# Kernel optimization log

Hardware: AMD Instinct MI355X
Metric: run time of the kernel (lower is better)

Reference implementation:

```python
import jax, jax.numpy as jnp
import numpy as np

N = 16384            # mesh vertices at full resolution (level 3)
DEG = 8              # avg nonzeros per Laplacian row
F_IN = 3
F_HID = 128
LOCAL_LAYERS = 15
LEVEL_N = [N >> (3 - l) for l in range(4)]  # [2048, 4096, 8192, 16384]


def setup_inputs():
    key = jax.random.key(0)
    ks = iter(jax.random.split(key, 48))
    d = {}
    d['inputs'] = jax.random.normal(next(ks), (1, N, F_IN), dtype=jnp.float32)
    d['mask0'] = jnp.ones((1, N, 1), jnp.float32)
    d['mask1'] = jnp.ones((1, N, 1), jnp.float32)
    for l, n in enumerate(LEVEL_N):
        e = DEG * n
        d[f'lap{l}_rows'] = jnp.sort(jax.random.randint(next(ks), (e,), 0, n, dtype=jnp.int32))
        d[f'lap{l}_cols'] = jax.random.randint(next(ks), (e,), 0, n, dtype=jnp.int32)
        d[f'lap{l}_vals'] = 0.25 * jax.random.normal(next(ks), (e,), dtype=jnp.float32)
    e = DEG * N
    d['L_rows'] = jnp.sort(jax.random.randint(next(ks), (e,), 0, N, dtype=jnp.int32))
    d['L_cols'] = jax.random.randint(next(ks), (e,), 0, N, dtype=jnp.int32)
    d['L_vals'] = 0.25 * jax.random.normal(next(ks), (e,), dtype=jnp.float32)
    s_in = 0.577   # ~1/sqrt(F_IN)
    s_h = 0.0625   # 1/sqrt(2*F_HID)
    d['g_conv1_W'] = s_in * jax.random.normal(next(ks), (F_IN, F_HID), dtype=jnp.float32)
    d['g_conv1_b'] = jnp.zeros((F_HID,), jnp.float32)
    d['g_down_W'] = s_h * jax.random.normal(next(ks), (3, 2, 2 * F_HID, F_HID), dtype=jnp.float32)
    d['g_down_b'] = jnp.zeros((3, 2, F_HID), jnp.float32)
    d['g_lap0_W'] = s_h * jax.random.normal(next(ks), (2, 2 * F_HID, F_HID), dtype=jnp.float32)
    d['g_lap0_b'] = jnp.zeros((2, F_HID), jnp.float32)
    d['g_up_W'] = s_h * jax.random.normal(next(ks), (3, 2, 2 * F_HID, F_HID), dtype=jnp.float32)
    d['g_up_b'] = jnp.zeros((3, 2, F_HID), jnp.float32)
    d['g_conv2_W'] = s_h * jax.random.normal(next(ks), (F_HID, 2), dtype=jnp.float32)
    d['g_conv2_b'] = jnp.zeros((2,), jnp.float32)
    d['l_conv1_W'] = s_in * jax.random.normal(next(ks), (F_IN, F_HID), dtype=jnp.float32)
    d['l_conv1_b'] = jnp.zeros((F_HID,), jnp.float32)
    d['l_rn_W'] = s_h * jax.random.normal(next(ks), (LOCAL_LAYERS, 2, 2 * F_HID, F_HID), dtype=jnp.float32)
    d['l_rn_b'] = jnp.zeros((LOCAL_LAYERS, 2, F_HID), jnp.float32)
    d['l_conv2_W'] = s_h * jax.random.normal(next(ks), (F_HID, 1), dtype=jnp.float32)
    d['l_conv2_b'] = jnp.zeros((1,), jnp.float32)
    return d


def _spmm(rows, cols, vals, x):
    # y = L @ x for an n x n COO Laplacian; x: [1, n, f] (batch=1, sparse mm path)
    y = jax.ops.segment_sum(vals[:, None] * x[0, cols, :], rows, num_segments=x.shape[1])
    return y[None]


def _lap_block(lap, x, Ws, bs):
    # _LapResNet2 (num_outputs == num_inputs == 128): elu -> cat([x, Lx]) -> 1x1 conv, residual
    inp = x
    for j in range(Ws.shape[0]):
        x = jax.nn.elu(x)
        x = jnp.concatenate([x, _spmm(lap[0], lap[1], lap[2], x)], axis=-1) @ Ws[j] + bs[j]
    return x + inp


def _avg_block(mask, x, Ws, bs):
    # _AvgResNet2: elu -> cat([x, masked global average]) -> 1x1 conv, residual
    inp = x
    denom = jnp.sum(mask, axis=1, keepdims=True)
    for j in range(Ws.shape[0]):
        x = jax.nn.elu(x)
        avg = jnp.sum(x * mask, axis=1, keepdims=True) / denom
        x = jnp.concatenate([x, jnp.broadcast_to(avg, x.shape)], axis=-1) @ Ws[j] + bs[j]
    return x + inp


def _maxpool2(x):
    # MaxPool1d(2, stride=2) along the node dim
    b, n, f = x.shape
    return x.reshape(b, n // 2, 2, f).max(axis=2)


def _forward(inputs, mask0, mask1, lap0_vals, lap1_vals, lap2_vals, lap3_vals, L_vals,
             g_conv1_W, g_conv1_b, g_down_W, g_down_b, g_lap0_W, g_lap0_b,
             g_up_W, g_up_b, g_conv2_W, g_conv2_b,
             l_conv1_W, l_conv1_b, l_rn_W, l_rn_b, l_conv2_W, l_conv2_b,
             lap0_rows, lap0_cols, lap1_rows, lap1_cols, lap2_rows, lap2_cols,
             lap3_rows, lap3_cols, L_rows, L_cols):
    laps = [(lap0_rows, lap0_cols, lap0_vals), (lap1_rows, lap1_cols, lap1_vals),
            (lap2_rows, lap2_cols, lap2_vals), (lap3_rows, lap3_cols, lap3_vals)]
    # ----- global net: EfficientCascade (naive max-pool cascade, 4 levels) -----
    # (mask0 is only max-pooled in torch; _LapResNet2 ignores it, so it does not affect math)
    x = inputs @ g_conv1_W + g_conv1_b
    down = []
    for k, i in enumerate((3, 2, 1)):
        down.append(x)
        x = _lap_block(laps[i], x, g_down_W[k], g_down_b[k])
        x = _maxpool2(x)
    x = _lap_block(laps[0], x, g_lap0_W, g_lap0_b)
    for i in (1, 2, 3):
        x = jnp.repeat(x, 2, axis=1)      # F.interpolate(scale_factor=2), nearest
        x = x + down[-i]                  # channels equal -> plain residual add
        x = _lap_block(laps[i], x, g_up_W[i - 1], g_up_b[i - 1])
    swg = jax.nn.elu(x) @ g_conv2_W + g_conv2_b + inputs[:, :, :2]  # + repeating_expand(inputs, 2)
    # ----- local net: LapDeepModel, 15 alternating Lap / global-avg resblocks -----
    L = (L_rows, L_cols, L_vals)
    y = inputs @ l_conv1_W + l_conv1_b
    for i in range(LOCAL_LAYERS):
        if i % 2 == 0:
            y = _lap_block(L, y, l_rn_W[i], l_rn_b[i])
        else:
            y = _avg_block(mask1, y, l_rn_W[i], l_rn_b[i])
    score_local = jax.nn.elu(y) @ l_conv2_W + l_conv2_b + inputs[:, :, :1]
    # ----- combine -----
    score_global = swg[:, :, :1]
    weight_global = jax.nn.sigmoid(swg[:, :, :-1])  # out_features=1 -> same first channel
    score_final = weight_global * score_global + (1.0 - weight_global) * score_local
    return jnp.concatenate([score_global, score_local, score_final], axis=1)


def reference(inputs, mask0, mask1, lap0_rows, lap0_cols, lap0_vals,
              lap1_rows, lap1_cols, lap1_vals, lap2_rows, lap2_cols, lap2_vals,
              lap3_rows, lap3_cols, lap3_vals, L_rows, L_cols, L_vals,
              g_conv1_W, g_conv1_b, g_down_W, g_down_b, g_lap0_W, g_lap0_b,
              g_up_W, g_up_b, g_conv2_W, g_conv2_b,
              l_conv1_W, l_conv1_b, l_rn_W, l_rn_b, l_conv2_W, l_conv2_b):
    return _forward(inputs, mask0, mask1, lap0_vals, lap1_vals, lap2_vals, lap3_vals, L_vals,
                    g_conv1_W, g_conv1_b, g_down_W, g_down_b, g_lap0_W, g_lap0_b,
                    g_up_W, g_up_b, g_conv2_W, g_conv2_b,
                    l_conv1_W, l_conv1_b, l_rn_W, l_rn_b, l_conv2_W, l_conv2_b,
                    lap0_rows, lap0_cols, lap1_rows, lap1_cols, lap2_rows, lap2_cols,
                    lap3_rows, lap3_cols, L_rows, L_cols)
```

## Files before the change

kernel.cpp:

```cpp
#include <hip/hip_runtime.h>

#define F 128
#define SPAD 136
#define NR 16

typedef __attribute__((ext_vector_type(8))) short short8;
typedef __attribute__((ext_vector_type(4))) float f32x4;
typedef unsigned long long ull;

__device__ __forceinline__ float elu_f(float x) {
    return x > 0.f ? x : __expf(x) - 1.f;
}
__device__ __forceinline__ ushort f2bf(float x) {
    unsigned u = __float_as_uint(x);
    u = (u + 0x7FFFu + ((u >> 16) & 1u)) >> 16;
    return (ushort)u;
}
__device__ __forceinline__ float bf2f(ushort u) {
    return __uint_as_float((unsigned)u << 16);
}
__device__ __forceinline__ void bfma8(float* a, float v, short8 u) {
#pragma unroll
    for (int i = 0; i < 8; ++i) a[i] += v * bf2f((ushort)u[i]);
}

struct SetupArgs {
    const float* ws0; const float* ws1; const float* ws2; const float* ws3;
    ushort* wd0; ushort* wd1; ushort* wd2; ushort* wd3;
    const int* rows0; const int* rows1; const int* rows2; const int* rows3; const int* rows4;
    int* rp0; int* rp1; int* rp2; int* rp3; int* rp4;
    const float* mask; float* den; float* acc;
    const float* in; const float* Wg; const float* bg; const float* Wl; const float* bl;
    ushort* og; ushort* eg; ushort* ol; ushort* el;
};

__global__ __launch_bounds__(256) void setup_conv1(SetupArgs s) {
    __shared__ ushort tile[16384];
    int b = blockIdx.x, t = threadIdx.x;
    if (b >= 274) {
        int id = (b - 274) * 256 + t;
        int r = id >> 7, c = id & 127;
        float x0 = s.in[r * 3 + 0], x1 = s.in[r * 3 + 1], x2 = s.in[r * 3 + 2];
        float g = x0 * s.Wg[c] + x1 * s.Wg[F + c] + x2 * s.Wg[2 * F + c] + s.bg[c];
        float lo = x0 * s.Wl[c] + x1 * s.Wl[F + c] + x2 * s.Wl[2 * F + c] + s.bl[c];
        s.og[id] = f2bf(g);  s.eg[id] = f2bf(elu_f(g));
        s.ol[id] = f2bf(lo); s.el[id] = f2bf(elu_f(lo));
    } else if (b < 88) {
        const float* src; ushort* dst; int lb;
        if (b < 12)      { src = s.ws0; dst = s.wd0; lb = b; }
        else if (b < 16) { src = s.ws1; dst = s.wd1; lb = b - 12; }
        else if (b < 28) { src = s.ws2; dst = s.wd2; lb = b - 16; }
        else             { src = s.ws3; dst = s.wd3; lb = b - 28; }
        src += (size_t)lb * 16384; dst += (size_t)lb * 16384;
        for (int idx = t; idx < 16384; idx += 256) {
            int k = idx >> 7, nn = idx & 127;
            int kt = k >> 5, lq = (k >> 3) & 3, j = k & 7;
            int wv = nn >> 5, ct = (nn >> 4) & 1, cc = nn & 15;
            tile[((((kt * 4 + wv) * 2 + ct) * 64 + lq * 16 + cc)) * 8 + j] = f2bf(src[idx]);
        }
        __syncthreads();
        ull* td = (ull*)dst; const ull* ts = (const ull*)tile;
        for (int i = t; i < 4096; i += 256) td[i] = ts[i];
    } else if (b < 273) {
        int tid = (b - 88) * 256 + t;
        const int ns[5] = {2048, 4096, 8192, 16384, 16384};
        const int es[5] = {16384, 32768, 65536, 131072, 131072};
        const int* rowsA[5] = {s.rows0, s.rows1, s.rows2, s.rows3, s.rows4};
        int* rpA[5] = {s.rp0, s.rp1, s.rp2, s.rp3, s.rp4};
        int base = 0;
        for (int lv = 0; lv < 5; ++lv) {
            int cnt = ns[lv] + 1;
            if (tid < base + cnt) {
                int r = tid - base;
                const int* rows = rowsA[lv]; int e = es[lv];
                int lo = 0, hi = e;
                while (lo < hi) { int mid = (lo + hi) >> 1; if (rows[mid] < r) lo = mid + 1; else hi = mid; }
                rpA[lv][r] = lo;
                return;
            }
            base += cnt;
        }
    } else {
        __shared__ float red[256];
        float ssum = 0.f;
        for (int i = t; i < 16384; i += 256) ssum += s.mask[i];
        red[t] = ssum; __syncthreads();
        for (int st = 128; st > 0; st >>= 1) { if (t < st) red[t] += red[t + st]; __syncthreads(); }
        if (t == 0) s.den[0] = red[0];
        for (int i = t; i < 14336; i += 256) s.acc[i] = 0.f;
    }
}

struct LArgs {
    const ushort* EA; const ushort* RES; ushort* OUT; ushort* EAOUT;
    const int* rowptr; const int* cols; const float* vals;
    const ushort* Wp; const float* bias;
    const float* accin; const float* den;
    const float* mask; float* accout;
    ushort* EO; ushort* EE; const ushort* SKIP;
    int epi;
    int fin;
    const float* Finp; const ushort* FEB0;
    const float* FgW2; const float* Fgb2; const float* FlW2; const float* Flb2;
    float* Fout;
};

__device__ __forceinline__ void layer_body(const LArgs& a, int blk, ushort* SS, float* FS) {
    const int t = threadIdx.x;
    const int rbase = blk * NR;
    const int w = t >> 6, l = t & 63;
    const int cl = l & 15, lq = l >> 4;
    const bool lap = (a.rowptr != nullptr);
    const bool avg = (a.accin != nullptr);

    if (lap) {
        const int grp = t >> 4, l16 = t & 15;
        const int lbase = l & ~15;
        const short8* EA8 = (const short8*)a.EA;
        const int row = rbase + grp;
        const int e0 = a.rowptr[row], e1 = a.rowptr[row + 1];
        float acc0[8];
#pragma unroll
        for (int i = 0; i < 8; ++i) acc0[i] = 0.f;
        int myc = 0; float myv = 0.f;
        if (e0 + l16 < e1) { myc = a.cols[e0 + l16]; myv = a.vals[e0 + l16]; }
#pragma unroll 1
        for (int base = e0; base < e1; base += 16) {
            int nc = 0; float nv = 0.f;
            {
                int en = base + 16 + l16;
                if (en < e1) { nc = a.cols[en]; nv = a.vals[en]; }
            }
#pragma unroll
            for (int half = 0; half < 2; ++half) {
                int hb = base + half * 8;
                if (hb < e1) {
                    int cnt = e1 - hb; if (cnt > 8) cnt = 8;
                    int cc[8];
#pragma unroll
                    for (int k = 0; k < 8; ++k) cc[k] = __shfl(myc, lbase + half * 8 + k, 64);
                    short8 ua[8];
#pragma unroll
                    for (int k = 0; k < 8; ++k)
                        if (k < cnt) ua[k] = EA8[(size_t)cc[k] * 16 + l16];
#pragma unroll
                    for (int k = 0; k < 8; ++k)
                        if (k < cnt) {
                            float v = __shfl(myv, lbase + half * 8 + k, 64);
                            bfma8(acc0, v, ua[k]);
                        }
                }
            }
            myc = nc; myv = nv;
        }
        short8 s0;
#pragma unroll
        for (int i = 0; i < 8; ++i) s0[i] = (short)f2bf(acc0[i]);
        *(short8*)(&SS[grp * SPAD + l16 * 8]) = s0;
        __syncthreads();
    } else if (avg) {
        if (t < 128) {
            float s = 0.f;
#pragma unroll
            for (int r = 0; r < 8; ++r) s += a.accin[r * 128 + t];
            SS[t] = f2bf(s / a.den[0]);
        }
        __syncthreads();
    }

    short8 afrag[4];
    {
        const ushort* ear = a.EA + (size_t)(rbase + cl) * F + lq * 8;
#pragma unroll
        for (int kt = 0; kt < 4; ++kt) afrag[kt] = *(const short8*)(ear + kt * 32);
    }

    f32x4 accA, accB;
#pragma unroll
    for (int i = 0; i < 4; ++i) { accA[i] = 0.f; accB[i] = 0.f; }
#pragma unroll
    for (int kt = 0; kt < 4; ++kt) {
        short8 b0 = *(const short8*)(a.Wp + (size_t)((((kt * 4 + w) * 2 + 0) * 64 + l) * 8));
        short8 b1 = *(const short8*)(a.Wp + (size_t)((((kt * 4 + w) * 2 + 1) * 64 + l) * 8));
        accA = __builtin_amdgcn_mfma_f32_16x16x32_bf16(afrag[kt], b0, accA, 0, 0, 0);
        accB = __builtin_amdgcn_mfma_f32_16x16x32_bf16(afrag[kt], b1, accB, 0, 0, 0);
    }
    if (lap || avg) {
        const ushort* esr = lap ? &SS[cl * SPAD + lq * 8] : &SS[lq * 8];
#pragma unroll
        for (int kt = 0; kt < 4; ++kt) {
            short8 aa = *(const short8*)(esr + kt * 32);
            short8 b0 = *(const short8*)(a.Wp + 16384 + (size_t)((((kt * 4 + w) * 2 + 0) * 64 + l) * 8));
            short8 b1 = *(const short8*)(a.Wp + 16384 + (size_t)((((kt * 4 + w) * 2 + 1) * 64 + l) * 8));
            accA = __builtin_amdgcn_mfma_f32_16x16x32_bf16(aa, b0, accA, 0, 0, 0);
            accB = __builtin_amdgcn_mfma_f32_16x16x32_bf16(aa, b1, accB, 0, 0, 0);
        }
    }

    const int col0 = w * 32 + cl, col1 = w * 32 + 16 + cl;
    const float bv0 = a.bias[col0], bv1 = a.bias[col1];
    float outv[8];
#pragma unroll
    for (int reg = 0; reg < 4; ++reg) {
        int r = lq * 4 + reg;
        size_t rg = (size_t)(rbase + r);
        float v0 = accA[reg] + bv0;
        float v1 = accB[reg] + bv1;
        if (a.RES) { v0 += bf2f(a.RES[rg * F + col0]); v1 += bf2f(a.RES[rg * F + col1]); }
        outv[reg] = v0; outv[4 + reg] = v1;
        if (a.OUT) { a.OUT[rg * F + col0] = f2bf(v0); a.OUT[rg * F + col1] = f2bf(v1); }
        if (a.EAOUT) { a.EAOUT[rg * F + col0] = f2bf(elu_f(v0)); a.EAOUT[rg * F + col1] = f2bf(elu_f(v1)); }
    }
    if (a.accout) {
        float p0 = 0.f, p1 = 0.f;
#pragma unroll
        for (int reg = 0; reg < 4; ++reg) {
            float mk = a.mask[rbase + lq * 4 + reg];
            p0 += elu_f(outv[reg]) * mk;
            p1 += elu_f(outv[4 + reg]) * mk;
        }
        p0 += __shfl_xor(p0, 16, 64); p0 += __shfl_xor(p0, 32, 64);
        p1 += __shfl_xor(p1, 16, 64); p1 += __shfl_xor(p1, 32, 64);
        if (l < 16) {
            atomicAdd(a.accout + (blk & 7) * 128 + w * 32 + l, p0);
            atomicAdd(a.accout + (blk & 7) * 128 + w * 32 + 16 + l, p1);
        }
    }
    if (a.epi == 1) {
        int rb2 = rbase >> 1;
#pragma unroll
        for (int ct = 0; ct < 2; ++ct)
#pragma unroll
            for (int e2 = 0; e2 < 2; ++e2) {
                float pv = fmaxf(outv[ct * 4 + e2 * 2], outv[ct * 4 + e2 * 2 + 1]);
                size_t idx = (size_t)(rb2 + lq * 2 + e2) * F + (ct ? col1 : col0);
                a.EO[idx] = f2bf(pv);
                a.EE[idx] = f2bf(elu_f(pv));
            }
    } else if (a.epi == 2) {
#pragma unroll
        for (int ct = 0; ct < 2; ++ct)
#pragma unroll
            for (int reg = 0; reg < 4; ++reg) {
                int r = lq * 4 + reg;
                size_t R0 = (size_t)(2 * (rbase + r)) * F + (ct ? col1 : col0);
                float v0 = outv[ct * 4 + reg] + bf2f(a.SKIP[R0]);
                float v1 = outv[ct * 4 + reg] + bf2f(a.SKIP[R0 + F]);
                a.EO[R0] = f2bf(v0);     a.EO[R0 + F] = f2bf(v1);
                a.EE[R0] = f2bf(elu_f(v0)); a.EE[R0 + F] = f2bf(elu_f(v1));
            }
    }
    if (a.fin) {
        __syncthreads();
        if (t < 32) FS[t] = 0.f;
        __syncthreads();
#pragma unroll
        for (int ct = 0; ct < 2; ++ct) {
            float lw = a.FlW2[ct ? col1 : col0];
#pragma unroll
            for (int reg = 0; reg < 4; ++reg)
                atomicAdd(&FS[lq * 4 + reg], elu_f(outv[ct * 4 + reg]) * lw);
        }
        for (int idx = t; idx < 16 * 128; idx += 256) {
            int r = idx >> 7, cc = idx & 127;
            atomicAdd(&FS[16 + r], bf2f(a.FEB0[(size_t)(rbase + r) * F + cc]) * a.FgW2[2 * cc]);
        }
        __syncthreads();
        if (t < 16) {
            int rg = rbase + t;
            float base = a.Finp[rg * 3 + 0];
            float sg = FS[16 + t] + a.Fgb2[0] + base;
            float sl = FS[t] + a.Flb2[0] + base;
            float wg = 1.f / (1.f + __expf(-sg));
            a.Fout[rg] = sg;
            a.Fout[16384 + rg] = sl;
            a.Fout[32768 + rg] = wg * sg + (1.f - wg) * sl;
        }
    }
}

__global__ __launch_bounds__(256)
void dual_layer(LArgs A, LArgs B, int nA) {
    __shared__ ushort SS[NR * SPAD];
    __shared__ float FS[64];
    bool isA = (int)blockIdx.x < nA;
    const LArgs& a = isA ? A : B;
    int blk = isA ? blockIdx.x : blockIdx.x - nA;
    layer_body(a, blk, SS, FS);
}

extern "C" void kernel_launch(void* const* d_in, const int* in_sizes, int n_in,
                              void* d_out, int out_size, void* d_ws, size_t ws_size,
                              hipStream_t stream) {
    (void)in_sizes; (void)n_in; (void)out_size; (void)ws_size;
    const float* inputs = (const float*)d_in[0];
    const float* mask1  = (const float*)d_in[2];
    const int*   lrows[5] = {(const int*)d_in[3], (const int*)d_in[6], (const int*)d_in[9],
                             (const int*)d_in[12], (const int*)d_in[15]};
    const int*   lcols[5] = {(const int*)d_in[4], (const int*)d_in[7], (const int*)d_in[10],
                             (const int*)d_in[13], (const int*)d_in[16]};
    const float* lvals[5] = {(const float*)d_in[5], (const float*)d_in[8], (const float*)d_in[11],
                             (const float*)d_in[14], (const float*)d_in[17]};
    const float* gW1 = (const float*)d_in[18];
    const float* gb1 = (const float*)d_in[19];
    const float* gdW = (const float*)d_in[20];
    const float* gdb = (const float*)d_in[21];
    const float* glW = (const float*)d_in[22];
    const float* glb = (const float*)d_in[23];
    const float* guW = (const float*)d_in[24];
    const float* gub = (const float*)d_in[25];
    const float* gW2 = (const float*)d_in[26];
    const float* gb2 = (const float*)d_in[27];
    const float* lW1 = (const float*)d_in[28];
    const float* lb1 = (const float*)d_in[29];
    const float* lrW = (const float*)d_in[30];
    const float* lrb = (const float*)d_in[31];
    const float* lW2 = (const float*)d_in[32];
    const float* lb2 = (const float*)d_in[33];
    float* out = (float*)d_out;

    const int N = 16384;
    const int nlev[5] = {2048, 4096, 8192, 16384, 16384};

    char* ws = (char*)d_ws;
    size_t off = 0;
    auto alloc = [&](size_t bytes) -> char* {
        char* p = ws + off;
        off = (off + bytes + 255) & ~(size_t)255;
        return p;
    };
    ushort* BUF0 = (ushort*)alloc((size_t)N * F * 2);
    ushort* GU2  = (ushort*)alloc((size_t)N * F * 2);
    ushort* G2   = (ushort*)alloc((size_t)N * F * 2);
    ushort* D8   = (ushort*)alloc((size_t)8192 * F * 2);
    ushort* D4   = (ushort*)alloc((size_t)4096 * F * 2);
    ushort* D2   = (ushort*)alloc((size_t)2048 * F * 2);
    ushort* LB   = (ushort*)alloc((size_t)N * F * 2);
    ushort* EB0 = (ushort*)alloc((size_t)N * F * 2);
    ushort* EG1 = (ushort*)alloc((size_t)N * F * 2);
    ushort* EG2 = (ushort*)alloc((size_t)N * F * 2);
    ushort* ED8 = (ushort*)alloc((size_t)8192 * F * 2);
    ushort* ED4 = (ushort*)alloc((size_t)4096 * F * 2);
    ushort* ED2 = (ushort*)alloc((size_t)2048 * F * 2);
    ushort* LE1 = (ushort*)alloc((size_t)N * F * 2);
    ushort* LE2 = (ushort*)alloc((size_t)N * F * 2);
    int* rp[5];
    for (int i = 0; i < 5; ++i) rp[i] = (int*)alloc((size_t)(nlev[i] + 1) * 4);
    float* ACC = (float*)alloc((size_t)14 * 8 * 128 * 4);
    float* DEN = (float*)alloc(4);
    ushort* Pd = (ushort*)alloc((size_t)12 * 16384 * 2);
    ushort* Pl = (ushort*)alloc((size_t)4  * 16384 * 2);
    ushort* Pu = (ushort*)alloc((size_t)12 * 16384 * 2);
    ushort* Pr = (ushort*)alloc((size_t)60 * 16384 * 2);

    SetupArgs sa;
    sa.ws0 = gdW; sa.ws1 = glW; sa.ws2 = guW; sa.ws3 = lrW;
    sa.wd0 = Pd;  sa.wd1 = Pl;  sa.wd2 = Pu;  sa.wd3 = Pr;
    sa.rows0 = lrows[0]; sa.rows1 = lrows[1]; sa.rows2 = lrows[2];
    sa.rows3 = lrows[3]; sa.rows4 = lrows[4];
    sa.rp0 = rp[0]; sa.rp1 = rp[1]; sa.rp2 = rp[2]; sa.rp3 = rp[3]; sa.rp4 = rp[4];
    sa.mask = mask1; sa.den = DEN; sa.acc = ACC;
    sa.in = inputs; sa.Wg = gW1; sa.bg = gb1; sa.Wl = lW1; sa.bl = lb1;
    sa.og = BUF0; sa.eg = EB0; sa.ol = LB; sa.el = LE1;
    setup_conv1<<<274 + 8192, 256, 0, stream>>>(sa);

    const size_t PSZ = 2 * 16384;

    auto mkL = [&](const ushort* ea, const ushort* res, ushort* o, ushort* eao,
                   int lv, const ushort* wp, const float* bias, float* accout,
                   int epi, ushort* eo, ushort* ee, const ushort* skip,
                   const float* accin, int fin) {
        LArgs x;
        x.EA = ea; x.RES = res; x.OUT = o; x.EAOUT = eao;
        x.rowptr = (lv >= 0) ? rp[lv] : nullptr;
        x.cols = (lv >= 0) ? lcols[lv] : nullptr;
        x.vals = (lv >= 0) ? lvals[lv] : nullptr;
        x.Wp = wp; x.bias = bias;
        x.accin = accin; x.den = DEN;
        x.mask = mask1; x.accout = accout;
        x.EO = eo; x.EE = ee; x.SKIP = skip; x.epi = epi;
        x.fin = fin;
        x.Finp = inputs; x.FEB0 = EB0;
        x.FgW2 = gW2; x.Fgb2 = gb2; x.FlW2 = lW2; x.Flb2 = lb2; x.Fout = out;
        return x;
    };

    LArgs gs[14]; int gn[14];
    gs[0]  = mkL(EB0, 0, 0, EG1, 3, Pd + 0 * PSZ, gdb + 0,   0, 0, 0, 0, 0, 0, 0);  gn[0]  = 16384;
    gs[1]  = mkL(EG1, BUF0, 0, 0, 3, Pd + 1 * PSZ, gdb + 128, 0, 1, D8, ED8, 0, 0, 0); gn[1] = 16384;
    gs[2]  = mkL(ED8, 0, 0, EG1, 2, Pd + 2 * PSZ, gdb + 256, 0, 0, 0, 0, 0, 0, 0);  gn[2]  = 8192;
    gs[3]  = mkL(EG1, D8, 0, 0, 2, Pd + 3 * PSZ, gdb + 384, 0, 1, D4, ED4, 0, 0, 0); gn[3]  = 8192;
    gs[4]  = mkL(ED4, 0, 0, EG1, 1, Pd + 4 * PSZ, gdb + 512, 0, 0, 0, 0, 0, 0, 0);  gn[4]  = 4096;
    gs[5]  = mkL(EG1, D4, 0, 0, 1, Pd + 5 * PSZ, gdb + 640, 0, 1, D2, ED2, 0, 0, 0); gn[5]  = 4096;
    gs[6]  = mkL(ED2, 0, 0, EG1, 0, Pl + 0 * PSZ, glb + 0,   0, 0, 0, 0, 0, 0, 0);  gn[6]  = 2048;
    gs[7]  = mkL(EG1, D2, 0, 0, 0, Pl + 1 * PSZ, glb + 128, 0, 2, GU2, EG2, D4, 0, 0); gn[7] = 2048;
    gs[8]  = mkL(EG2, 0, 0, EG1, 1, Pu + 0 * PSZ, gub + 0,   0, 0, 0, 0, 0, 0, 0);  gn[8]  = 4096;
    gs[9]  = mkL(EG1, GU2, 0, 0, 1, Pu + 1 * PSZ, gub + 128, 0, 2, G2, EG2, D8, 0, 0); gn[9] = 4096;
    gs[10] = mkL(EG2, 0, 0, EG1, 2, Pu + 2 * PSZ, gub + 256, 0, 0, 0, 0, 0, 0, 0);  gn[10] = 8192;
    gs[11] = mkL(EG1, G2, 0, 0, 2, Pu + 3 * PSZ, gub + 384, 0, 2, GU2, EG2, BUF0, 0, 0); gn[11] = 8192;
    gs[12] = mkL(EG2, 0, 0, EG1, 3, Pu + 4 * PSZ, gub + 512, 0, 0, 0, 0, 0, 0, 0);  gn[12] = 16384;
    gs[13] = mkL(EG1, GU2, 0, EB0, 3, Pu + 5 * PSZ, gub + 640, 0, 0, 0, 0, 0, 0, 0); gn[13] = 16384;

    const int NB_LOC = N / NR;
    int gi = 0;
    auto launchLap = [&](const LArgs& loc) {
        if (gi < 14) {
            int na = gn[gi] / NR;
            dual_layer<<<na + NB_LOC, 256, 0, stream>>>(gs[gi], loc, na);
            ++gi;
        } else {
            dual_layer<<<NB_LOC, 256, 0, stream>>>(loc, loc, NB_LOC);
        }
    };

    for (int i = 0; i < 15; ++i) {
        const ushort* P1 = Pr + (size_t)(2 * i) * PSZ;
        const ushort* P2 = Pr + (size_t)(2 * i + 1) * PSZ;
        const float* b1 = lrb + (size_t)i * 256;
        const float* b2 = b1 + 128;
        if ((i & 1) == 0) {
            LArgs s1 = mkL(LE1, 0, 0, LE2, 4, P1, b1, 0, 0, 0, 0, 0, 0, 0);
            float* accout = (i <= 12) ? (ACC + (size_t)i * 1024) : nullptr;
            int fin = (i == 14);
            LArgs s2 = mkL(LE2, LB, fin ? nullptr : LB, fin ? nullptr : LE1, 4,
                           P2, b2, accout, 0, 0, 0, 0, 0, fin);
            launchLap(s1);
            launchLap(s2);
        } else {
            LArgs s1 = mkL(LE1, 0, 0, LE2, -1, P1, b1, ACC + (size_t)i * 1024,
                           0, 0, 0, 0, ACC + (size_t)(i - 1) * 1024, 0);
            LArgs s2 = mkL(LE2, LB, LB, LE1, -1, P2, b2, 0,
                           0, 0, 0, 0, ACC + (size_t)i * 1024, 0);
            launchLap(s1);
            launchLap(s2);
        }
    }
}
```

Baseline: 596.0 us.

## Sort full-resolution Laplacian rows by degree to balance per-block SpMM work

Adds a small kernel that builds a permutation of the 16384-row level-3 and local Laplacian rows, bucketed by nonzero count in descending order. The affected global and local layers then process rows in that order and gather and scatter through the permutation for activations, residuals, mask and final outputs. The aim is that rows sharing a block and wavefront have similar edge counts, so fewer lanes sit idle in the gather loop. The cost is one extra launch, an indirection load per row, and row accesses that are no longer contiguous across a block.

```diff
diff --git a/kernel.cpp b/kernel.cpp
--- a/kernel.cpp
+++ b/kernel.cpp
@@ -91,9 +91,38 @@
     }
 }
 
+struct PermArgs { const int* rpA; int* permA; const int* rpB; int* permB; int n; };
+
+__global__ __launch_bounds__(1024) void build_perm(PermArgs p) {
+    const int* rp = blockIdx.x ? p.rpB : p.rpA;
+    int* perm = blockIdx.x ? p.permB : p.permA;
+    const int n = p.n;
+    __shared__ int hist[64];
+    __shared__ int base[64];
+    int t = threadIdx.x;
+    if (t < 64) hist[t] = 0;
+    __syncthreads();
+    for (int r = t; r < n; r += 1024) {
+        int d = rp[r + 1] - rp[r]; if (d > 63) d = 63;
+        atomicAdd(&hist[d], 1);
+    }
+    __syncthreads();
+    if (t == 0) {
+        int acc = 0;
+        for (int d = 63; d >= 0; --d) { base[d] = acc; acc += hist[d]; }
+    }
+    __syncthreads();
+    for (int r = t; r < n; r += 1024) {
+        int d = rp[r + 1] - rp[r]; if (d > 63) d = 63;
+        int pos = atomicAdd(&base[d], 1);
+        perm[pos] = r;
+    }
+}
+
 struct LArgs {
     const ushort* EA; const ushort* RES; ushort* OUT; ushort* EAOUT;
     const int* rowptr; const int* cols; const float* vals;
+    const int* perm;
     const ushort* Wp; const float* bias;
     const float* accin; const float* den;
     const float* mask; float* accout;
@@ -112,12 +141,13 @@
     const int cl = l & 15, lq = l >> 4;
     const bool lap = (a.rowptr != nullptr);
     const bool avg = (a.accin != nullptr);
+    const int* pm = a.perm;
 
     if (lap) {
         const int grp = t >> 4, l16 = t & 15;
         const int lbase = l & ~15;
         const short8* EA8 = (const short8*)a.EA;
-        const int row = rbase + grp;
+        const int row = pm ? pm[rbase + grp] : (rbase + grp);
         const int e0 = a.rowptr[row], e1 = a.rowptr[row + 1];
         float acc0[8];
 #pragma unroll
@@ -170,7 +200,8 @@
 
     short8 afrag[4];
     {
-        const ushort* ear = a.EA + (size_t)(rbase + cl) * F + lq * 8;
+        const int rowA = pm ? pm[rbase + cl] : (rbase + cl);
+        const ushort* ear = a.EA + (size_t)rowA * F + lq * 8;
 #pragma unroll
         for (int kt = 0; kt < 4; ++kt) afrag[kt] = *(const short8*)(ear + kt * 32);
     }
@@ -203,7 +234,7 @@
 #pragma unroll
     for (int reg = 0; reg < 4; ++reg) {
         int r = lq * 4 + reg;
-        size_t rg = (size_t)(rbase + r);
+        size_t rg = (size_t)(pm ? pm[rbase + r] : (rbase + r));
         float v0 = accA[reg] + bv0;
         float v1 = accB[reg] + bv1;
         if (a.RES) { v0 += bf2f(a.RES[rg * F + col0]); v1 += bf2f(a.RES[rg * F + col1]); }
@@ -215,7 +246,9 @@
         float p0 = 0.f, p1 = 0.f;
 #pragma unroll
         for (int reg = 0; reg < 4; ++reg) {
-            float mk = a.mask[rbase + lq * 4 + reg];
+            int r = lq * 4 + reg;
+            int rg = pm ? pm[rbase + r] : (rbase + r);
+            float mk = a.mask[rg];
             p0 += elu_f(outv[reg]) * mk;
             p1 += elu_f(outv[4 + reg]) * mk;
         }
@@ -263,11 +296,12 @@
         }
         for (int idx = t; idx < 16 * 128; idx += 256) {
             int r = idx >> 7, cc = idx & 127;
-            atomicAdd(&FS[16 + r], bf2f(a.FEB0[(size_t)(rbase + r) * F + cc]) * a.FgW2[2 * cc]);
+            int rg = pm ? pm[rbase + r] : (rbase + r);
+            atomicAdd(&FS[16 + r], bf2f(a.FEB0[(size_t)rg * F + cc]) * a.FgW2[2 * cc]);
         }
         __syncthreads();
         if (t < 16) {
-            int rg = rbase + t;
+            int rg = pm ? pm[rbase + t] : (rbase + t);
             float base = a.Finp[rg * 3 + 0];
             float sg = FS[16 + t] + a.Fgb2[0] + base;
             float sl = FS[t] + a.Flb2[0] + base;
@@ -348,6 +382,8 @@
     for (int i = 0; i < 5; ++i) rp[i] = (int*)alloc((size_t)(nlev[i] + 1) * 4);
     float* ACC = (float*)alloc((size_t)14 * 8 * 128 * 4);
     float* DEN = (float*)alloc(4);
+    int* P3 = (int*)alloc((size_t)N * 4);
+    int* P4 = (int*)alloc((size_t)N * 4);
     ushort* Pd = (ushort*)alloc((size_t)12 * 16384 * 2);
     ushort* Pl = (ushort*)alloc((size_t)4  * 16384 * 2);
     ushort* Pu = (ushort*)alloc((size_t)12 * 16384 * 2);
@@ -364,6 +400,12 @@
     sa.og = BUF0; sa.eg = EB0; sa.ol = LB; sa.el = LE1;
     setup_conv1<<<274 + 8192, 256, 0, stream>>>(sa);
 
+    PermArgs pa;
+    pa.rpA = rp[3]; pa.permA = P3;
+    pa.rpB = rp[4]; pa.permB = P4;
+    pa.n = N;
+    build_perm<<<2, 1024, 0, stream>>>(pa);
+
     const size_t PSZ = 2 * 16384;
 
     auto mkL = [&](const ushort* ea, const ushort* res, ushort* o, ushort* eao,
@@ -375,6 +417,7 @@
         x.rowptr = (lv >= 0) ? rp[lv] : nullptr;
         x.cols = (lv >= 0) ? lcols[lv] : nullptr;
         x.vals = (lv >= 0) ? lvals[lv] : nullptr;
+        x.perm = nullptr;
         x.Wp = wp; x.bias = bias;
         x.accin = accin; x.den = DEN;
         x.mask = mask1; x.accout = accout;
@@ -400,6 +443,7 @@
     gs[11] = mkL(EG1, G2, 0, 0, 2, Pu + 3 * PSZ, gub + 384, 0, 2, GU2, EG2, BUF0, 0, 0); gn[11] = 8192;
     gs[12] = mkL(EG2, 0, 0, EG1, 3, Pu + 4 * PSZ, gub + 512, 0, 0, 0, 0, 0, 0, 0);  gn[12] = 16384;
     gs[13] = mkL(EG1, GU2, 0, EB0, 3, Pu + 5 * PSZ, gub + 640, 0, 0, 0, 0, 0, 0, 0); gn[13] = 16384;
+    gs[0].perm = P3; gs[12].perm = P3; gs[13].perm = P3;
 
     const int NB_LOC = N / NR;
     int gi = 0;
@@ -420,10 +464,12 @@
         const float* b2 = b1 + 128;
         if ((i & 1) == 0) {
             LArgs s1 = mkL(LE1, 0, 0, LE2, 4, P1, b1, 0, 0, 0, 0, 0, 0, 0);
+            s1.perm = P4;
             float* accout = (i <= 12) ? (ACC + (size_t)i * 1024) : nullptr;
             int fin = (i == 14);
             LArgs s2 = mkL(LE2, LB, fin ? nullptr : LB, fin ? nullptr : LE1, 4,
                            P2, b2, accout, 0, 0, 0, 0, 0, fin);
+            s2.perm = P4;
             launchLap(s1);
             launchLap(s2);
         } else {
```

Measured after the change: 663.3 us. 1.11x slower.

## Fuse paired avg-pool residual layers into one kernel with a grid-wide barrier

Applied to the files above, without the earlier changes.

For odd local layers, the two launches (first half producing the masked mean, second half consuming it) are merged into one fused kernel. Blocks spin on an agent-scope atomic counter until every local block has added its partial sums, then run the second GEMM from shared memory. This removes a kernel launch and a global round trip of the intermediate activation per pair, and it co-schedules global-branch blocks in the same grid. It relies on all NB_LOC blocks being resident at once, otherwise the spin barrier deadlocks. Counters are zeroed in the setup kernel.

```diff
diff --git a/kernel.cpp b/kernel.cpp
--- a/kernel.cpp
+++ b/kernel.cpp
@@ -30,6 +30,7 @@
     const int* rows0; const int* rows1; const int* rows2; const int* rows3; const int* rows4;
     int* rp0; int* rp1; int* rp2; int* rp3; int* rp4;
     const float* mask; float* den; float* acc;
+    int* cnt;
     const float* in; const float* Wg; const float* bg; const float* Wl; const float* bl;
     ushort* og; ushort* eg; ushort* ol; ushort* el;
 };
@@ -88,6 +89,7 @@
         for (int st = 128; st > 0; st >>= 1) { if (t < st) red[t] += red[t + st]; __syncthreads(); }
         if (t == 0) s.den[0] = red[0];
         for (int i = t; i < 14336; i += 256) s.acc[i] = 0.f;
+        for (int i = t; i < 112; i += 256) s.cnt[i] = 0;
     }
 }
 
@@ -287,6 +289,140 @@
     const LArgs& a = isA ? A : B;
     int blk = isA ? blockIdx.x : blockIdx.x - nA;
     layer_body(a, blk, SS, FS);
+}
+
+struct AvgArgs {
+    const ushort* EA;
+    ushort* EAOUT;
+    const ushort* LBin;
+    ushort* LBout;
+    const ushort* W1; const ushort* W2;
+    const float* b1; const float* b2;
+    const float* accin;
+    float* accmid;
+    const float* den; const float* mask;
+    int* cnt;
+};
+
+__device__ __forceinline__ void avg_fused_body(const AvgArgs& a, int blk, int nLoc,
+                                               ushort* SS, ushort* AV) {
+    const int t = threadIdx.x;
+    const int rbase = blk * NR;
+    const int w = t >> 6, l = t & 63;
+    const int cl = l & 15, lq = l >> 4;
+    const int col0 = w * 32 + cl, col1 = col0 + 16;
+
+    if (t < 128) {
+        float s = 0.f;
+#pragma unroll
+        for (int r = 0; r < 8; ++r) s += a.accin[r * 128 + t];
+        AV[t] = f2bf(s / a.den[0]);
+    }
+    short8 afrag[4];
+    {
+        const ushort* ear = a.EA + (size_t)(rbase + cl) * F + lq * 8;
+#pragma unroll
+        for (int kt = 0; kt < 4; ++kt) afrag[kt] = *(const short8*)(ear + kt * 32);
+    }
+    __syncthreads();
+
+    f32x4 accA, accB;
+#pragma unroll
+    for (int i = 0; i < 4; ++i) { accA[i] = 0.f; accB[i] = 0.f; }
+#pragma unroll
+    for (int kt = 0; kt < 4; ++kt) {
+        short8 b0 = *(const short8*)(a.W1 + (size_t)((((kt * 4 + w) * 2 + 0) * 64 + l) * 8));
+        short8 b1 = *(const short8*)(a.W1 + (size_t)((((kt * 4 + w) * 2 + 1) * 64 + l) * 8));
+        accA = __builtin_amdgcn_mfma_f32_16x16x32_bf16(afrag[kt], b0, accA, 0, 0, 0);
+        accB = __builtin_amdgcn_mfma_f32_16x16x32_bf16(afrag[kt], b1, accB, 0, 0, 0);
+        short8 aa = *(const short8*)(&AV[lq * 8] + kt * 32);
+        short8 c0 = *(const short8*)(a.W1 + 16384 + (size_t)((((kt * 4 + w) * 2 + 0) * 64 + l) * 8));
+        short8 c1 = *(const short8*)(a.W1 + 16384 + (size_t)((((kt * 4 + w) * 2 + 1) * 64 + l) * 8));
+        accA = __builtin_amdgcn_mfma_f32_16x16x32_bf16(aa, c0, accA, 0, 0, 0);
+        accB = __builtin_amdgcn_mfma_f32_16x16x32_bf16(aa, c1, accB, 0, 0, 0);
+    }
+    {
+        const float bv0 = a.b1[col0], bv1 = a.b1[col1];
+        float p0 = 0.f, p1 = 0.f;
+#pragma unroll
+        for (int reg = 0; reg < 4; ++reg) {
+            int r = lq * 4 + reg;
+            float e0 = elu_f(accA[reg] + bv0);
+            float e1 = elu_f(accB[reg] + bv1);
+            float mk = a.mask[rbase + r];
+            p0 += e0 * mk; p1 += e1 * mk;
+            SS[r * SPAD + col0] = f2bf(e0);
+            SS[r * SPAD + col1] = f2bf(e1);
+        }
+        p0 += __shfl_xor(p0, 16, 64); p0 += __shfl_xor(p0, 32, 64);
+        p1 += __shfl_xor(p1, 16, 64); p1 += __shfl_xor(p1, 32, 64);
+        if (l < 16) {
+            atomicAdd(a.accmid + (blk & 7) * 128 + w * 32 + l, p0);
+            atomicAdd(a.accmid + (blk & 7) * 128 + w * 32 + 16 + l, p1);
+        }
+    }
+
+    __syncthreads();
+    if (t == 0) {
+        __hip_atomic_fetch_add(a.cnt, 1, __ATOMIC_ACQ_REL, __HIP_MEMORY_SCOPE_AGENT);
+        while (__hip_atomic_load(a.cnt, __ATOMIC_ACQUIRE, __HIP_MEMORY_SCOPE_AGENT) < nLoc)
+            __builtin_amdgcn_s_sleep(2);
+    }
+    __syncthreads();
+
+    if (t < 128) {
+        float s = 0.f;
+#pragma unroll
+        for (int r = 0; r < 8; ++r)
+            s += __hip_atomic_load(a.accmid + r * 128 + t, __ATOMIC_RELAXED,
+                                   __HIP_MEMORY_SCOPE_AGENT);
+        AV[t] = f2bf(s / a.den[0]);
+    }
+    short8 af2[4];
+    {
+        const ushort* esr = &SS[cl * SPAD + lq * 8];
+#pragma unroll
+        for (int kt = 0; kt < 4; ++kt) af2[kt] = *(const short8*)(esr + kt * 32);
+    }
+    __syncthreads();
+
+#pragma unroll
+    for (int i = 0; i < 4; ++i) { accA[i] = 0.f; accB[i] = 0.f; }
+#pragma unroll
+    for (int kt = 0; kt < 4; ++kt) {
+        short8 b0 = *(const short8*)(a.W2 + (size_t)((((kt * 4 + w) * 2 + 0) * 64 + l) * 8));
+        short8 b1 = *(const short8*)(a.W2 + (size_t)((((kt * 4 + w) * 2 + 1) * 64 + l) * 8));
+        accA = __builtin_amdgcn_mfma_f32_16x16x32_bf16(af2[kt], b0, accA, 0, 0, 0);
+        accB = __builtin_amdgcn_mfma_f32_16x16x32_bf16(af2[kt], b1, accB, 0, 0, 0);
+        short8 aa = *(const short8*)(&AV[lq * 8] + kt * 32);
+        short8 c0 = *(const short8*)(a.W2 + 16384 + (size_t)((((kt * 4 + w) * 2 + 0) * 64 + l) * 8));
+        short8 c1 = *(const short8*)(a.W2 + 16384 + (size_t)((((kt * 4 + w) * 2 + 1) * 64 + l) * 8));
+        accA = __builtin_amdgcn_mfma_f32_16x16x32_bf16(aa, c0, accA, 0, 0, 0);
+        accB = __builtin_amdgcn_mfma_f32_16x16x32_bf16(aa, c1, accB, 0, 0, 0);
+    }
+    {
+        const float bv0 = a.b2[col0], bv1 = a.b2[col1];
+#pragma unroll
+        for (int reg = 0; reg < 4; ++reg) {
+            int r = lq * 4 + reg;
+            size_t rg = (size_t)(rbase + r);
+            float v0 = accA[reg] + bv0 + bf2f(a.LBin[rg * F + col0]);
+            float v1 = accB[reg] + bv1 + bf2f(a.LBin[rg * F + col1]);
+            a.LBout[rg * F + col0] = f2bf(v0);
+            a.LBout[rg * F + col1] = f2bf(v1);
+            a.EAOUT[rg * F + col0] = f2bf(elu_f(v0));
+            a.EAOUT[rg * F + col1] = f2bf(elu_f(v1));
+        }
+    }
+}
+
+__global__ __launch_bounds__(256, 8)
+void dual_avg(LArgs G, AvgArgs V, int nA, int nLoc) {
+    __shared__ ushort SS[NR * SPAD];
+    __shared__ ushort AV[128];
+    __shared__ float FS[64];
+    if ((int)blockIdx.x < nA) layer_body(G, blockIdx.x, SS, FS);
+    else avg_fused_body(V, (int)blockIdx.x - nA, nLoc, SS, AV);
 }
 
 extern "C" void kernel_launch(void* const* d_in, const int* in_sizes, int n_in,
@@ -348,6 +484,7 @@
     for (int i = 0; i < 5; ++i) rp[i] = (int*)alloc((size_t)(nlev[i] + 1) * 4);
     float* ACC = (float*)alloc((size_t)14 * 8 * 128 * 4);
     float* DEN = (float*)alloc(4);
+    int* CNT = (int*)alloc((size_t)7 * 16 * 4);
     ushort* Pd = (ushort*)alloc((size_t)12 * 16384 * 2);
     ushort* Pl = (ushort*)alloc((size_t)4  * 16384 * 2);
     ushort* Pu = (ushort*)alloc((size_t)12 * 16384 * 2);
@@ -359,7 +496,7 @@
     sa.rows0 = lrows[0]; sa.rows1 = lrows[1]; sa.rows2 = lrows[2];
     sa.rows3 = lrows[3]; sa.rows4 = lrows[4];
     sa.rp0 = rp[0]; sa.rp1 = rp[1]; sa.rp2 = rp[2]; sa.rp3 = rp[3]; sa.rp4 = rp[4];
-    sa.mask = mask1; sa.den = DEN; sa.acc = ACC;
+    sa.mask = mask1; sa.den = DEN; sa.acc = ACC; sa.cnt = CNT;
     sa.in = inputs; sa.Wg = gW1; sa.bg = gb1; sa.Wl = lW1; sa.bl = lb1;
     sa.og = BUF0; sa.eg = EB0; sa.ol = LB; sa.el = LE1;
     setup_conv1<<<274 + 8192, 256, 0, stream>>>(sa);
@@ -427,12 +564,22 @@
             launchLap(s1);
             launchLap(s2);
         } else {
-            LArgs s1 = mkL(LE1, 0, 0, LE2, -1, P1, b1, ACC + (size_t)i * 1024,
-                           0, 0, 0, 0, ACC + (size_t)(i - 1) * 1024, 0);
-            LArgs s2 = mkL(LE2, LB, LB, LE1, -1, P2, b2, 0,
-                           0, 0, 0, 0, ACC + (size_t)i * 1024, 0);
-            launchLap(s1);
-            launchLap(s2);
-        }
-    }
-}
+            AvgArgs v;
+            v.EA = LE1; v.EAOUT = LE1;
+            v.LBin = LB; v.LBout = LB;
+            v.W1 = P1; v.W2 = P2;
+            v.b1 = b1; v.b2 = b2;
+            v.accin = ACC + (size_t)(i - 1) * 1024;
+            v.accmid = ACC + (size_t)i * 1024;
+            v.den = DEN; v.mask = mask1;
+            v.cnt = CNT + (size_t)(i >> 1) * 16;
+            if (gi < 14) {
+                int na = gn[gi] / NR;
+                dual_avg<<<na + NB_LOC, 256, 0, stream>>>(gs[gi], v, na, NB_LOC);
+                ++gi;
+            } else {
+                dual_avg<<<NB_LOC, 256, 0, stream>>>(gs[0], v, 0, NB_LOC);
+            }
+        }
+    }
+}
```

Result: slower. 1.319 ms (+121.3%).
